# Kernel optimization log

Hardware: AMD Instinct MI355X
Metric: run time of the kernel (lower is better)

## Reference

```python
import jax, jax.numpy as jnp
import numpy as np

EMBED_DIM = 1024
NUM_HEADS = 16
D_K = EMBED_DIM // NUM_HEADS
BATCH, SEQ = 4, 2048


def setup_inputs() -> dict:
    key = jax.random.key(0)
    ks = jax.random.split(key, 6)
    s = 1.0 / np.sqrt(EMBED_DIM)
    return {
        "x": jax.random.normal(ks[0], (BATCH, SEQ, EMBED_DIM), dtype=jnp.float32),
        "mask": jnp.ones((BATCH, SEQ), dtype=jnp.int32),
        "Wq": jax.random.uniform(ks[1], (EMBED_DIM, EMBED_DIM), jnp.float32, -s, s),
        "Wk": jax.random.uniform(ks[2], (EMBED_DIM, EMBED_DIM), jnp.float32, -s, s),
        "Wv": jax.random.uniform(ks[3], (EMBED_DIM, EMBED_DIM), jnp.float32, -s, s),
        "Wo": jax.random.uniform(ks[4], (EMBED_DIM, EMBED_DIM), jnp.float32, -s, s),
    }


def reference(x, mask, Wq, Wk, Wv, Wo):
    B, S, E = x.shape
    H, Dk = NUM_HEADS, D_K
    # nn.Linear: y = x @ W.T ; reshape to [B, H, S, Dk]
    def proj(W):
        return jnp.einsum('bse,fe->bsf', x, W).reshape(B, S, H, Dk).transpose(0, 2, 1, 3)
    q, k, v = proj(Wq), proj(Wk), proj(Wv)
    scores = jnp.einsum('bhqd,bhkd->bhqk', q, k) / jnp.sqrt(jnp.float32(Dk))
    # key-padding mask: [B, S] -> [B, 1, 1, S]; 0 means masked with -inf
    scores = jnp.where(mask[:, None, None, :] == 0, -jnp.inf, scores)
    attn = jax.nn.softmax(scores, axis=-1)  # dropout is identity (p=0 / eval)
    out = jnp.einsum('bhqk,bhkd->bhqd', attn, v)
    out = out.transpose(0, 2, 1, 3).reshape(B, S, E)
    return jnp.einsum('bse,fe->bsf', out, Wo)
```

## Files before the change

### kernel.cpp

```cpp
#include <hip/hip_runtime.h>

typedef __attribute__((ext_vector_type(8))) __bf16   bf16x8;
typedef __attribute__((ext_vector_type(8))) _Float16 f16x8;
typedef __attribute__((ext_vector_type(2))) __fp16   h16x2;
typedef __attribute__((ext_vector_type(8))) __fp16   h16x8;
typedef __attribute__((ext_vector_type(4))) float    f32x4;

#define MFMA_BF16 __builtin_amdgcn_mfma_f32_16x16x32_bf16
#define MFMA_F16  __builtin_amdgcn_mfma_f32_16x16x32_f16

__global__ __launch_bounds__(256)
void prep_all(const float* __restrict__ x,  const float* __restrict__ Wq,
              const float* __restrict__ Wk, const float* __restrict__ Wv,
              const float* __restrict__ Wo, const int* __restrict__ mask,
              __bf16* __restrict__ xh, __bf16* __restrict__ w3,
              __bf16* __restrict__ wo, float* __restrict__ bias)
{
    const int i = blockIdx.x * 256 + threadIdx.x;

    if (i < 1572864) {
        const float* src; __bf16* dst; int o8;
        if (i < 1048576)      { src = x;  dst = xh;            o8 = i; }
        else if (i < 1179648) { src = Wq; dst = w3;            o8 = i - 1048576; }
        else if (i < 1310720) { src = Wk; dst = w3 + 1048576;  o8 = i - 1179648; }
        else if (i < 1441792) { src = Wv; dst = w3 + 2097152;  o8 = i - 1310720; }
        else                  { src = Wo; dst = wo;            o8 = i - 1441792; }
        float4 v0 = *(const float4*)(src + (size_t)o8 * 8);
        float4 v1 = *(const float4*)(src + (size_t)o8 * 8 + 4);
        float xs[8] = {v0.x, v0.y, v0.z, v0.w, v1.x, v1.y, v1.z, v1.w};
        bf16x8 h8;
        #pragma unroll
        for (int jj = 0; jj < 8; jj++) h8[jj] = (__bf16)xs[jj];
        *(bf16x8*)(dst + (size_t)o8 * 8) = h8;
    } else {
        int c = i - 1572864;
        int4 m0 = *(const int4*)(mask + c * 8);
        int4 m1 = *(const int4*)(mask + c * 8 + 4);
        float4 b0, b1;
        b0.x = m0.x ? 0.f : -30000.f;  b0.y = m0.y ? 0.f : -30000.f;
        b0.z = m0.z ? 0.f : -30000.f;  b0.w = m0.w ? 0.f : -30000.f;
        b1.x = m1.x ? 0.f : -30000.f;  b1.y = m1.y ? 0.f : -30000.f;
        b1.z = m1.z ? 0.f : -30000.f;  b1.w = m1.w ? 0.f : -30000.f;
        *(float4*)(bias + c * 8)     = b0;
        *(float4*)(bias + c * 8 + 4) = b1;
    }
}

#define GEMM_DECLS                                                          \
    __shared__ __bf16 Ah[128][40], Bh[128][40];                             \
    const int t    = threadIdx.x;                                           \
    const int lane = t & 63;                                                \
    const int wid  = t >> 6;                                                \
    const int l15  = lane & 15;                                             \
    const int lg   = lane >> 4;                                             \
    const int wr   = wid >> 1, wc = wid & 1;

#define GEMM_LOOP(Ag, Bg, m0, brow0, K)                                     \
    f32x4 acc[4][4];                                                        \
    _Pragma("unroll")                                                       \
    for (int i = 0; i < 4; i++)                                             \
        _Pragma("unroll")                                                   \
        for (int jj = 0; jj < 4; jj++)                                      \
            _Pragma("unroll")                                               \
            for (int r = 0; r < 4; r++) acc[i][jj][r] = 0.f;                \
    for (int k0 = 0; k0 < K; k0 += 32) {                                    \
        __syncthreads();                                                    \
        _Pragma("unroll")                                                   \
        for (int i = 0; i < 2; i++) {                                       \
            int id = t + 256 * i;                                           \
            int row = id >> 2, cc = id & 3;                                 \
            *(bf16x8*)&Ah[row][cc*8] =                                      \
                *(const bf16x8*)(Ag + (size_t)(m0 + row) * K + k0 + cc*8);  \
            *(bf16x8*)&Bh[row][cc*8] =                                      \
                *(const bf16x8*)(Bg + (size_t)(brow0 + row) * K + k0 + cc*8);\
        }                                                                   \
        __syncthreads();                                                    \
        bf16x8 ah[4];                                                       \
        _Pragma("unroll")                                                   \
        for (int mr = 0; mr < 4; mr++)                                      \
            ah[mr] = *(const bf16x8*)&Ah[wr*64 + mr*16 + l15][lg*8];        \
        _Pragma("unroll")                                                   \
        for (int nr = 0; nr < 4; nr++) {                                    \
            bf16x8 bh = *(const bf16x8*)&Bh[wc*64 + nr*16 + l15][lg*8];     \
            _Pragma("unroll")                                               \
            for (int mr = 0; mr < 4; mr++)                                  \
                acc[mr][nr] = MFMA_BF16(ah[mr], bh, acc[mr][nr], 0, 0, 0);  \
        }                                                                   \
    }

__global__ __launch_bounds__(256, 4)
void gemm_qkv(const __bf16* __restrict__ xh, const __bf16* __restrict__ w3,
              __bf16* __restrict__ qh, __bf16* __restrict__ kh,
              _Float16* __restrict__ vh)
{
    GEMM_DECLS
    const int K = 1024, N = 1024;
    const int m0     = blockIdx.x * 128;
    const int by     = blockIdx.y;
    const int region = by >> 3;
    const int n0     = (by & 7) * 128;
    const int brow0  = region * 1024 + n0;
    GEMM_LOOP(xh, w3, m0, brow0, K)

    constexpr float QSCALE = 0.18033688011112f;
    #pragma unroll
    for (int mr = 0; mr < 4; mr++)
    #pragma unroll
    for (int r = 0; r < 4; r++) {
        int row = m0 + wr*64 + mr*16 + lg*4 + r;
        #pragma unroll
        for (int nr = 0; nr < 4; nr++) {
            int col = n0 + wc*64 + nr*16 + l15;
            size_t off = (size_t)row * N + col;
            float v = acc[mr][nr][r];
            if (region == 0)      qh[off] = (__bf16)(v * QSCALE);
            else if (region == 1) kh[off] = (__bf16)v;
            else                  vh[off] = (_Float16)v;
        }
    }
}

__global__ __launch_bounds__(256, 4)
void gemm_out(const __bf16* __restrict__ aoh, const __bf16* __restrict__ woh,
              float* __restrict__ out, int M, int N, int K)
{
    GEMM_DECLS
    const int m0 = blockIdx.x * 128, n0 = blockIdx.y * 128;
    GEMM_LOOP(aoh, woh, m0, n0, K)

    #pragma unroll
    for (int mr = 0; mr < 4; mr++)
    #pragma unroll
    for (int r = 0; r < 4; r++) {
        int row = m0 + wr*64 + mr*16 + lg*4 + r;
        #pragma unroll
        for (int nr = 0; nr < 4; nr++) {
            int col = n0 + wc*64 + nr*16 + l15;
            out[(size_t)row * N + col] = acc[mr][nr][r];
        }
    }
}

__global__ __launch_bounds__(256, 2)
void attn_bf16(const __bf16* __restrict__ Qg, const __bf16* __restrict__ Kg,
               const _Float16* __restrict__ Vg, const float* __restrict__ biasg,
               __bf16* AO)
{
    const int S = 2048, E = 1024;
    __shared__ __align__(16) char smem[36864];

    const int tid  = threadIdx.x;
    const int lane = tid & 63;
    const int wid  = tid >> 6;
    const int l15  = lane & 15;
    const int lg   = lane >> 4;

    const int fid = blockIdx.x;
    const int xcd = fid & 7;
    const int j   = fid >> 3;
    const int bh  = xcd * 8 + (j >> 4);
    const int qb  = j & 15;
    const int h   = bh & 15;
    const int b   = bh >> 4;
    const int q0  = qb * 128;
    const size_t base = (size_t)b * S * E + (size_t)h * 64;

    bf16x8 qf[2][2];
    #pragma unroll
    for (int mg = 0; mg < 2; mg++) {
        size_t qoff = base + (size_t)(q0 + wid*32 + mg*16 + l15) * E;
        #pragma unroll
        for (int kc = 0; kc < 2; kc++)
            qf[mg][kc] = *(const bf16x8*)(Qg + qoff + kc*32 + lg*8);
    }

    f32x4 o[2][4], osum[2];
    #pragma unroll
    for (int mg = 0; mg < 2; mg++) {
        #pragma unroll
        for (int nt = 0; nt < 4; nt++)
            #pragma unroll
            for (int r = 0; r < 4; r++) o[mg][nt][r] = 0.f;
        #pragma unroll
        for (int r = 0; r < 4; r++) osum[mg][r] = 0.f;
    }

    f16x8 ones8;
    #pragma unroll
    for (int jj = 0; jj < 8; jj++) ones8[jj] = (_Float16)1.0f;

    const int srow0 = tid >> 3;
    const int srow1 = srow0 + 32;
    const int scc   = tid & 7;
    const int sg0   = ((srow0 & 12) >> 2) * 8 + ((srow0 >> 4) & 1) * 4
                    + (srow0 & 3) + (srow0 & 32);
    const int sg1   = ((srow1 & 12) >> 2) * 8 + ((srow1 >> 4) & 1) * 4
                    + (srow1 & 3) + (srow1 & 32);
    const int colw0 = (((sg0 >> 3) ^ scc) << 3) + (sg0 & 7);
    const int colw1 = (((sg1 >> 3) ^ scc) << 3) + (sg1 & 7);

    bf16x8 kpre0, kpre1; f16x8 vpre0, vpre1;
    {
        size_t ga = base + (size_t)srow0 * E + scc * 8;
        size_t gb = base + (size_t)srow1 * E + scc * 8;
        kpre0 = *(const bf16x8*)(Kg + ga);  vpre0 = *(const f16x8*)(Vg + ga);
        kpre1 = *(const bf16x8*)(Kg + gb);  vpre1 = *(const f16x8*)(Vg + gb);
    }

    const int NT = S / 64;
    f16x8 pa_prev[2][2];

    {
        __bf16   (*Kh)[72] = (__bf16 (*)[72])smem;
        _Float16 (*Vt)[72] = (_Float16 (*)[72])(smem + 9216);
        *(bf16x8*)&Kh[srow0][scc*8] = kpre0;
        *(bf16x8*)&Kh[srow1][scc*8] = kpre1;
        #pragma unroll
        for (int jj = 0; jj < 8; jj++) Vt[scc*8 + jj][colw0] = vpre0[jj];
        #pragma unroll
        for (int jj = 0; jj < 8; jj++) Vt[scc*8 + jj][colw1] = vpre1[jj];
        {
            size_t ga = base + (size_t)(64 + srow0) * E + scc * 8;
            size_t gb = base + (size_t)(64 + srow1) * E + scc * 8;
            kpre0 = *(const bf16x8*)(Kg + ga);  vpre0 = *(const f16x8*)(Vg + ga);
            kpre1 = *(const bf16x8*)(Kg + gb);  vpre1 = *(const f16x8*)(Vg + gb);
        }
        __syncthreads();

        f32x4 sf[2][4];
        #pragma unroll
        for (int kvb = 0; kvb < 4; kvb++) {
            f32x4 bias4 = *(const f32x4*)(biasg + b * S + kvb*16 + lg*4);
            sf[0][kvb] = bias4;  sf[1][kvb] = bias4;
        }
        #pragma unroll
        for (int kc = 0; kc < 2; kc++)
            #pragma unroll
            for (int kvb = 0; kvb < 4; kvb++) {
                bf16x8 kb = *(const bf16x8*)&Kh[kvb*16 + l15][kc*32 + lg*8];
                #pragma unroll
                for (int mg = 0; mg < 2; mg++)
                    sf[mg][kvb] = MFMA_BF16(kb, qf[mg][kc], sf[mg][kvb], 0, 0, 0);
            }
        #pragma unroll
        for (int mg = 0; mg < 2; mg++) {
            float p[4][4];
            #pragma unroll
            for (int kvb = 0; kvb < 4; kvb++)
                #pragma unroll
                for (int r = 0; r < 4; r++)
                    p[kvb][r] = __builtin_amdgcn_exp2f(sf[mg][kvb][r]);
            #pragma unroll
            for (int hh = 0; hh < 2; hh++) {
                h16x2 c0 = __builtin_amdgcn_cvt_pkrtz(p[2*hh][0],   p[2*hh][1]);
                h16x2 c1 = __builtin_amdgcn_cvt_pkrtz(p[2*hh][2],   p[2*hh][3]);
                h16x2 c2 = __builtin_amdgcn_cvt_pkrtz(p[2*hh+1][0], p[2*hh+1][1]);
                h16x2 c3 = __builtin_amdgcn_cvt_pkrtz(p[2*hh+1][2], p[2*hh+1][3]);
                h16x8 t8 = __builtin_shufflevector(
                    __builtin_shufflevector(c0, c1, 0, 1, 2, 3),
                    __builtin_shufflevector(c2, c3, 0, 1, 2, 3),
                    0, 1, 2, 3, 4, 5, 6, 7);
                pa_prev[mg][hh] = __builtin_bit_cast(f16x8, t8);
            }
        }
    }

    for (int t = 1; t < NT; t++) {
        const int k0 = t * 64;
        char* bufc = smem + (t & 1) * 18432;
        char* bufp = smem + ((t - 1) & 1) * 18432;
        __bf16   (*Kh)[72]  = (__bf16 (*)[72])bufc;
        _Float16 (*Vt)[72]  = (_Float16 (*)[72])(bufc + 9216);
        _Float16 (*Vtp)[72] = (_Float16 (*)[72])(bufp + 9216);

        __syncthreads();
        *(bf16x8*)&Kh[srow0][scc*8] = kpre0;
        *(bf16x8*)&Kh[srow1][scc*8] = kpre1;
        #pragma unroll
        for (int jj = 0; jj < 8; jj++) Vt[scc*8 + jj][colw0] = vpre0[jj];
        #pragma unroll
        for (int jj = 0; jj < 8; jj++) Vt[scc*8 + jj][colw1] = vpre1[jj];

        if (t + 1 < NT) {
            size_t ga = base + (size_t)(k0 + 64 + srow0) * E + scc * 8;
            size_t gb = base + (size_t)(k0 + 64 + srow1) * E + scc * 8;
            kpre0 = *(const bf16x8*)(Kg + ga);  vpre0 = *(const f16x8*)(Vg + ga);
            kpre1 = *(const bf16x8*)(Kg + gb);  vpre1 = *(const f16x8*)(Vg + gb);
        }
        __syncthreads();

        f32x4 sf[2][4];
        #pragma unroll
        for (int kvb = 0; kvb < 4; kvb++) {
            f32x4 bias4 = *(const f32x4*)(biasg + b * S + k0 + kvb*16 + lg*4);
            sf[0][kvb] = bias4;  sf[1][kvb] = bias4;
        }
        #pragma unroll
        for (int kc = 0; kc < 2; kc++)
            #pragma unroll
            for (int kvb = 0; kvb < 4; kvb++) {
                bf16x8 kb = *(const bf16x8*)&Kh[kvb*16 + l15][kc*32 + lg*8];
                #pragma unroll
                for (int mg = 0; mg < 2; mg++)
                    sf[mg][kvb] = MFMA_BF16(kb, qf[mg][kc], sf[mg][kvb], 0, 0, 0);
            }

        #pragma unroll
        for (int hh = 0; hh < 2; hh++) {
            #pragma unroll
            for (int nt = 0; nt < 4; nt++) {
                int c8p = (hh*4 + lg) ^ (nt*2 + (l15 >> 3));
                f16x8 vb = *(const f16x8*)&Vtp[nt*16 + l15][c8p*8];
                o[0][nt] = MFMA_F16(pa_prev[0][hh], vb, o[0][nt], 0, 0, 0);
                o[1][nt] = MFMA_F16(pa_prev[1][hh], vb, o[1][nt], 0, 0, 0);
            }
            osum[0] = MFMA_F16(pa_prev[0][hh], ones8, osum[0], 0, 0, 0);
            osum[1] = MFMA_F16(pa_prev[1][hh], ones8, osum[1], 0, 0, 0);
        }

        #pragma unroll
        for (int mg = 0; mg < 2; mg++) {
            float p[4][4];
            #pragma unroll
            for (int kvb = 0; kvb < 4; kvb++)
                #pragma unroll
                for (int r = 0; r < 4; r++)
                    p[kvb][r] = __builtin_amdgcn_exp2f(sf[mg][kvb][r]);
            #pragma unroll
            for (int hh = 0; hh < 2; hh++) {
                h16x2 c0 = __builtin_amdgcn_cvt_pkrtz(p[2*hh][0],   p[2*hh][1]);
                h16x2 c1 = __builtin_amdgcn_cvt_pkrtz(p[2*hh][2],   p[2*hh][3]);
                h16x2 c2 = __builtin_amdgcn_cvt_pkrtz(p[2*hh+1][0], p[2*hh+1][1]);
                h16x2 c3 = __builtin_amdgcn_cvt_pkrtz(p[2*hh+1][2], p[2*hh+1][3]);
                h16x8 t8 = __builtin_shufflevector(
                    __builtin_shufflevector(c0, c1, 0, 1, 2, 3),
                    __builtin_shufflevector(c2, c3, 0, 1, 2, 3),
                    0, 1, 2, 3, 4, 5, 6, 7);
                pa_prev[mg][hh] = __builtin_bit_cast(f16x8, t8);
            }
        }
    }

    {
        char* bufp = smem + ((NT - 1) & 1) * 18432;
        _Float16 (*Vtp)[72] = (_Float16 (*)[72])(bufp + 9216);
        #pragma unroll
        for (int hh = 0; hh < 2; hh++) {
            #pragma unroll
            for (int nt = 0; nt < 4; nt++) {
                int c8p = (hh*4 + lg) ^ (nt*2 + (l15 >> 3));
                f16x8 vb = *(const f16x8*)&Vtp[nt*16 + l15][c8p*8];
                o[0][nt] = MFMA_F16(pa_prev[0][hh], vb, o[0][nt], 0, 0, 0);
                o[1][nt] = MFMA_F16(pa_prev[1][hh], vb, o[1][nt], 0, 0, 0);
            }
            osum[0] = MFMA_F16(pa_prev[0][hh], ones8, osum[0], 0, 0, 0);
            osum[1] = MFMA_F16(pa_prev[1][hh], ones8, osum[1], 0, 0, 0);
        }
    }

    float inv[2][4];
    #pragma unroll
    for (int mg = 0; mg < 2; mg++)
        #pragma unroll
        for (int r = 0; r < 4; r++) inv[mg][r] = 1.0f / osum[mg][r];

    unsigned short* Pu = (unsigned short*)smem;
    __syncthreads();
    #pragma unroll
    for (int mg = 0; mg < 2; mg++)
        #pragma unroll
        for (int r = 0; r < 4; r++)
            #pragma unroll
            for (int nt = 0; nt < 4; nt++) {
                __bf16 v = (__bf16)(o[mg][nt][r] * inv[mg][r]);
                Pu[(wid*32 + mg*16 + lg*4 + r) * 72 + nt*16 + l15] =
                    *(unsigned short*)&v;
            }
    __syncthreads();
    #pragma unroll
    for (int i = 0; i < 4; i++) {
        int u   = tid + 256 * i;
        int row = u >> 3, c8 = u & 7;
        bf16x8 v8;
        #pragma unroll
        for (int jj = 0; jj < 8; jj++) {
            unsigned short us = Pu[row * 72 + c8*8 + jj];
            v8[jj] = *(__bf16*)&us;
        }
        *(bf16x8*)(AO + base + (size_t)(q0 + row) * E + c8 * 8) = v8;
    }
}

extern "C" void kernel_launch(void* const* d_in, const int* in_sizes, int n_in,
                              void* d_out, int out_size, void* d_ws, size_t ws_size,
                              hipStream_t stream)
{
    const float* x    = (const float*)d_in[0];
    const int*   mask = (const int*)  d_in[1];
    const float* Wq   = (const float*)d_in[2];
    const float* Wk   = (const float*)d_in[3];
    const float* Wv   = (const float*)d_in[4];
    const float* Wo   = (const float*)d_in[5];
    float* out = (float*)d_out;

    const int B = 4, S = 2048, E = 1024;
    const int M = B * S;
    const size_t SZ  = (size_t)M * E;
    const size_t WSZ = (size_t)E * E;
    const size_t PB  = SZ * sizeof(__bf16);

    char* ws = (char*)d_ws;
    __bf16*   qh = (__bf16*)(ws);
    __bf16*   kh = (__bf16*)(ws + PB);
    _Float16* vh = (_Float16*)(ws + 2*PB);
    __bf16*   xh = (__bf16*)(ws + 3*PB);
    __bf16*   w3 = (__bf16*)(ws + 4*PB);
    __bf16*   wo = (__bf16*)(ws + 4*PB + 3*WSZ*sizeof(__bf16));
    float*    bs = (float*)(ws + 4*PB + 4*WSZ*sizeof(__bf16));

    prep_all<<<dim3(6148), dim3(256), 0, stream>>>(
        x, Wq, Wk, Wv, Wo, mask, xh, w3, wo, bs);

    gemm_qkv<<<dim3(M/128, 24), dim3(256), 0, stream>>>(xh, w3, qh, kh, vh);

    attn_bf16<<<dim3(1024), dim3(256), 0, stream>>>(qh, kh, vh, bs, qh);

    gemm_out<<<dim3(M/128, E/128), dim3(256), 0, stream>>>(qh, wo, out, M, E, E);
}
```

Measured before the change: 197.8 us.

## Register-prefetch next GEMM tile and remap blocks for XCD-aware L2 locality

Both projection GEMMs now load the next K-slice of A and B into registers while the current slice is consumed from shared memory, so global-load latency overlaps with MFMA work. The grids become 1D and are remapped so blocks landing on the same XCD share weight columns (QKV) or the same output tile column (out projection), aiming for better L2 reuse. Launch bounds drop from 4 to 3 waves per SIMD to leave room for the extra prefetch registers, which may lower occupancy.

Result: slower. 203.7 us (+3.0%).

```diff
diff --git a/kernel.cpp b/kernel.cpp
--- a/kernel.cpp
+++ b/kernel.cpp
@@ -53,9 +53,11 @@
     const int wid  = t >> 6;                                                \
     const int l15  = lane & 15;                                             \
     const int lg   = lane >> 4;                                             \
-    const int wr   = wid >> 1, wc = wid & 1;
-
-#define GEMM_LOOP(Ag, Bg, m0, brow0, K)                                     \
+    const int wr   = wid >> 1, wc = wid & 1;                                \
+    const int srow0 = t >> 2, srow1 = (t >> 2) + 64;                        \
+    const int scc8  = (t & 3) * 8;
+
+#define GEMM_LOOP_DB(Ag, Bg, m0, brow0, K)                                  \
     f32x4 acc[4][4];                                                        \
     _Pragma("unroll")                                                       \
     for (int i = 0; i < 4; i++)                                             \
@@ -63,16 +65,22 @@
         for (int jj = 0; jj < 4; jj++)                                      \
             _Pragma("unroll")                                               \
             for (int r = 0; r < 4; r++) acc[i][jj][r] = 0.f;                \
+    bf16x8 ar0, ar1, br0, br1;                                              \
+    ar0 = *(const bf16x8*)(Ag + (size_t)(m0 + srow0) * K + scc8);           \
+    ar1 = *(const bf16x8*)(Ag + (size_t)(m0 + srow1) * K + scc8);           \
+    br0 = *(const bf16x8*)(Bg + (size_t)(brow0 + srow0) * K + scc8);        \
+    br1 = *(const bf16x8*)(Bg + (size_t)(brow0 + srow1) * K + scc8);        \
     for (int k0 = 0; k0 < K; k0 += 32) {                                    \
         __syncthreads();                                                    \
-        _Pragma("unroll")                                                   \
-        for (int i = 0; i < 2; i++) {                                       \
-            int id = t + 256 * i;                                           \
-            int row = id >> 2, cc = id & 3;                                 \
-            *(bf16x8*)&Ah[row][cc*8] =                                      \
-                *(const bf16x8*)(Ag + (size_t)(m0 + row) * K + k0 + cc*8);  \
-            *(bf16x8*)&Bh[row][cc*8] =                                      \
-                *(const bf16x8*)(Bg + (size_t)(brow0 + row) * K + k0 + cc*8);\
+        *(bf16x8*)&Ah[srow0][scc8] = ar0;                                   \
+        *(bf16x8*)&Ah[srow1][scc8] = ar1;                                   \
+        *(bf16x8*)&Bh[srow0][scc8] = br0;                                   \
+        *(bf16x8*)&Bh[srow1][scc8] = br1;                                   \
+        if (k0 + 32 < K) {                                                  \
+            ar0 = *(const bf16x8*)(Ag + (size_t)(m0 + srow0) * K + k0+32 + scc8);   \
+            ar1 = *(const bf16x8*)(Ag + (size_t)(m0 + srow1) * K + k0+32 + scc8);   \
+            br0 = *(const bf16x8*)(Bg + (size_t)(brow0 + srow0) * K + k0+32 + scc8);\
+            br1 = *(const bf16x8*)(Bg + (size_t)(brow0 + srow1) * K + k0+32 + scc8);\
         }                                                                   \
         __syncthreads();                                                    \
         bf16x8 ah[4];                                                       \
@@ -88,19 +96,22 @@
         }                                                                   \
     }
 
-__global__ __launch_bounds__(256, 4)
+__global__ __launch_bounds__(256, 3)
 void gemm_qkv(const __bf16* __restrict__ xh, const __bf16* __restrict__ w3,
               __bf16* __restrict__ qh, __bf16* __restrict__ kh,
               _Float16* __restrict__ vh)
 {
     GEMM_DECLS
     const int K = 1024, N = 1024;
-    const int m0     = blockIdx.x * 128;
-    const int by     = blockIdx.y;
+    const int wg  = blockIdx.x;
+    const int xcd = wg & 7;
+    const int j   = wg >> 3;
+    const int by  = xcd * 3 + (j >> 6);
+    const int m0  = (j & 63) * 128;
     const int region = by >> 3;
     const int n0     = (by & 7) * 128;
     const int brow0  = region * 1024 + n0;
-    GEMM_LOOP(xh, w3, m0, brow0, K)
+    GEMM_LOOP_DB(xh, w3, m0, brow0, K)
 
     constexpr float QSCALE = 0.18033688011112f;
     #pragma unroll
@@ -120,13 +131,16 @@
     }
 }
 
-__global__ __launch_bounds__(256, 4)
+__global__ __launch_bounds__(256, 3)
 void gemm_out(const __bf16* __restrict__ aoh, const __bf16* __restrict__ woh,
-              float* __restrict__ out, int M, int N, int K)
+              float* __restrict__ out)
 {
     GEMM_DECLS
-    const int m0 = blockIdx.x * 128, n0 = blockIdx.y * 128;
-    GEMM_LOOP(aoh, woh, m0, n0, K)
+    const int K = 1024, N = 1024;
+    const int wg  = blockIdx.x;
+    const int n0  = (wg & 7) * 128;
+    const int m0  = (wg >> 3) * 128;
+    GEMM_LOOP_DB(aoh, woh, m0, n0, K)
 
     #pragma unroll
     for (int mr = 0; mr < 4; mr++)
@@ -421,9 +435,9 @@
     prep_all<<<dim3(6148), dim3(256), 0, stream>>>(
         x, Wq, Wk, Wv, Wo, mask, xh, w3, wo, bs);
 
-    gemm_qkv<<<dim3(M/128, 24), dim3(256), 0, stream>>>(xh, w3, qh, kh, vh);
+    gemm_qkv<<<dim3(1536), dim3(256), 0, stream>>>(xh, w3, qh, kh, vh);
 
     attn_bf16<<<dim3(1024), dim3(256), 0, stream>>>(qh, kh, vh, bs, qh);
 
-    gemm_out<<<dim3(M/128, E/128), dim3(256), 0, stream>>>(qh, wo, out, M, E, E);
+    gemm_out<<<dim3(512), dim3(256), 0, stream>>>(qh, wo, out);
 }
```
